# Kernel optimization log

Measured on AMD Instinct MI355X. Metric: run time of the kernel, lower is better.

Reference implementation:

```python
import jax, jax.numpy as jnp
import numpy as np

B, S, D = 2, 2048, 2048
H, HD = 16, 128
F = 8192
LC = 512
EPS = 1e-6


def _linear_params(k, din, dout):
    k1, k2 = jax.random.split(k)
    w = jax.random.normal(k1, (din, dout), jnp.float32) * 0.02
    b = jax.random.normal(k2, (dout,), jnp.float32) * 0.02
    return w, b


def setup_inputs() -> dict:
    key = jax.random.key(0)
    ks = jax.random.split(key, 20)
    inp = {}
    inp["x"] = jax.random.normal(ks[0], (B, S, D), jnp.float32)
    inp["e"] = jax.random.normal(ks[1], (B, 6, D), jnp.float32) * 0.1
    inp["context"] = jax.random.normal(ks[2], (B, LC, D), jnp.float32)
    # per-token rotary angles [S, HD//2] (Wan builds such a table from 3D grid)
    inp["freqs"] = jax.random.uniform(ks[3], (S, HD // 2), jnp.float32) * (2.0 * np.pi)
    inp["modulation"] = jax.random.normal(ks[4], (1, 6, D), jnp.float32) / np.sqrt(D)
    names = ["sq", "sk", "sv", "so", "cq", "ck", "cv", "co"]
    for i, nm in enumerate(names):
        w, b = _linear_params(ks[5 + i], D, D)
        inp[nm + "_w"], inp[nm + "_b"] = w, b
    inp["f1_w"], inp["f1_b"] = _linear_params(ks[13], D, F)
    inp["f2_w"], inp["f2_b"] = _linear_params(ks[14], F, D)
    inp["snq"] = jnp.ones((D,), jnp.float32)
    inp["snk"] = jnp.ones((D,), jnp.float32)
    inp["cnq"] = jnp.ones((D,), jnp.float32)
    inp["cnk"] = jnp.ones((D,), jnp.float32)
    return inp


def _rmsnorm(x, w):
    # WanRMSNorm: x * rsqrt(mean(x^2) + eps) * weight
    return x * jax.lax.rsqrt(jnp.mean(x * x, axis=-1, keepdims=True) + EPS) * w


def _layernorm(x):
    # elementwise_affine=False LayerNorm
    m = jnp.mean(x, axis=-1, keepdims=True)
    v = jnp.mean((x - m) ** 2, axis=-1, keepdims=True)
    return (x - m) * jax.lax.rsqrt(v + EPS)


def _rope(x, ang):
    # x: [B, S, H, HD]; ang: [S, HD//2]; adjacent pairs rotated (view_as_complex)
    c = jnp.cos(ang)[None, :, None, :]
    s = jnp.sin(ang)[None, :, None, :]
    xr, xi = x[..., 0::2], x[..., 1::2]
    out = jnp.stack([xr * c - xi * s, xr * s + xi * c], axis=-1)
    return out.reshape(x.shape)


def _attn(q, k, v):
    # q: [B,Sq,H,HD], k/v: [B,Sk,H,HD] -> [B,Sq,H,HD]
    scores = jnp.einsum("bqhd,bkhd->bhqk", q, k) / np.sqrt(HD)
    probs = jax.nn.softmax(scores, axis=-1)
    return jnp.einsum("bhqk,bkhd->bqhd", probs, v)


def reference(x, e, context, freqs, modulation,
              sq_w, sq_b, sk_w, sk_b, sv_w, sv_b, so_w, so_b, snq, snk,
              cq_w, cq_b, ck_w, ck_b, cv_w, cv_b, co_w, co_b, cnq, cnk,
              f1_w, f1_b, f2_w, f2_b):
    em = modulation + e  # [B,6,D]
    e0, e1, e2, e3, e4, e5 = [em[:, i:i + 1, :] for i in range(6)]

    # self-attention with AdaLN modulation
    tx = _layernorm(x) * (1.0 + e1) + e0
    q = _rmsnorm(tx @ sq_w + sq_b, snq).reshape(B, S, H, HD)
    k = _rmsnorm(tx @ sk_w + sk_b, snk).reshape(B, S, H, HD)
    v = (tx @ sv_w + sv_b).reshape(B, S, H, HD)
    q, k = _rope(q, freqs), _rope(k, freqs)
    y = _attn(q, k, v).reshape(B, S, D) @ so_w + so_b
    x = x + y * e2

    # cross-attention (norm3 = Identity since cross_attn_norm=False)
    q = _rmsnorm(x @ cq_w + cq_b, cnq).reshape(B, S, H, HD)
    k = _rmsnorm(context @ ck_w + ck_b, cnk).reshape(B, LC, H, HD)
    v = (context @ cv_w + cv_b).reshape(B, LC, H, HD)
    x = x + (_attn(q, k, v).reshape(B, S, D) @ co_w + co_b)

    # FFN with AdaLN modulation
    tx = _layernorm(x) * (1.0 + e4) + e3
    y = jax.nn.gelu(tx @ f1_w + f1_b, approximate=True) @ f2_w + f2_b
    x = x + y * e5
    return x
```

## Files before the change

kernel.cpp:

```cpp
#include <hip/hip_runtime.h>
#include <hip/hip_bf16.h>

using bf16 = __hip_bfloat16;
typedef __attribute__((ext_vector_type(8))) short bf16x8;
typedef __attribute__((ext_vector_type(4))) float f32x4;
typedef const __attribute__((address_space(1))) unsigned int* gp_t;
typedef __attribute__((address_space(3))) unsigned int* sp_t;

#define B_   2
#define S_   2048
#define D_   2048
#define H_   16
#define HD_  128
#define F_   8192
#define LC_  512
#define ESTRIDE (6*D_)

__device__ __forceinline__ float bsum4(float v, float* rs) {
  #pragma unroll
  for (int o = 32; o; o >>= 1) v += __shfl_down(v, o, 64);
  int lane = threadIdx.x & 63, w = threadIdx.x >> 6;
  if (!lane) rs[w] = v;
  __syncthreads();
  float r = rs[0] + rs[1] + rs[2] + rs[3];
  __syncthreads();
  return r;
}
__device__ __forceinline__ float bmax4(float v, float* rs) {
  #pragma unroll
  for (int o = 32; o; o >>= 1) v = fmaxf(v, __shfl_down(v, o, 64));
  int lane = threadIdx.x & 63, w = threadIdx.x >> 6;
  if (!lane) rs[w] = v;
  __syncthreads();
  float r = fmaxf(fmaxf(rs[0], rs[1]), fmaxf(rs[2], rs[3]));
  __syncthreads();
  return r;
}

template <int N>
__device__ __forceinline__ void vmwait() {
  asm volatile("s_waitcnt vmcnt(%0)" :: "n"(N) : "memory");
}
__device__ __forceinline__ void vmnone() {}

__global__ void k_addmod(const float* __restrict__ e, const float* __restrict__ mod,
                         float* __restrict__ em) {
  int i = blockIdx.x * 256 + threadIdx.x;
  em[i] = e[i] + mod[i % (6 * D_)];
}

__global__ void k_f2b(const float* __restrict__ in, bf16* __restrict__ out) {
  int i = blockIdx.x * 256 + threadIdx.x;
  out[i] = __float2bfloat16(in[i]);
}

__global__ void k_copy_f32(const float* __restrict__ in, float* __restrict__ out) {
  int i = blockIdx.x * 256 + threadIdx.x;
  out[i] = in[i];
}

__global__ void k_tr_f2b(const float* __restrict__ in, bf16* __restrict__ out,
                         int K, int N) {
  __shared__ float tile[64][65];
  int kb = blockIdx.y << 6, nb = blockIdx.x << 6;
  int x = threadIdx.x & 63, y = threadIdx.x >> 6;
  #pragma unroll
  for (int r = y; r < 64; r += 4) tile[r][x] = in[(size_t)(kb + r) * N + nb + x];
  __syncthreads();
  #pragma unroll
  for (int r = y; r < 64; r += 4)
    out[(size_t)(nb + r) * K + kb + x] = __float2bfloat16(tile[x][r]);
}

__global__ void k_tr_b2b(const bf16* __restrict__ in, bf16* __restrict__ out,
                         int R, int C, long long sIn, long long sOut) {
  in  += (long long)blockIdx.z * sIn;
  out += (long long)blockIdx.z * sOut;
  __shared__ bf16 tile[64][65];
  int rb = blockIdx.y << 6, cb = blockIdx.x << 6;
  int x = threadIdx.x & 63, y = threadIdx.x >> 6;
  #pragma unroll
  for (int r = y; r < 64; r += 4) tile[r][x] = in[(size_t)(rb + r) * C + cb + x];
  __syncthreads();
  #pragma unroll
  for (int r = y; r < 64; r += 4) out[(size_t)(cb + r) * R + rb + x] = tile[x][r];
}

__global__ void k_ln_mod(const float* __restrict__ x, const float* __restrict__ em,
                         int i0, int i1, bf16* __restrict__ out, int s_per_b) {
  __shared__ float rs[4];
  int row = blockIdx.x, t = threadIdx.x;
  int b = row / s_per_b;
  const float* xr = x + (size_t)row * D_;
  float vals[8], s = 0.f, ss = 0.f;
  #pragma unroll
  for (int j = 0; j < 8; j++) {
    float v = xr[t + j * 256];
    vals[j] = v; s += v; ss += v * v;
  }
  s  = bsum4(s, rs);
  ss = bsum4(ss, rs);
  float mean = s * (1.f / D_);
  float var  = ss * (1.f / D_) - mean * mean;
  float inv  = rsqrtf(var + 1e-6f);
  const float* e0 = em + ((size_t)b * 6 + i0) * D_;
  const float* e1 = em + ((size_t)b * 6 + i1) * D_;
  bf16* orow = out + (size_t)row * D_;
  #pragma unroll
  for (int j = 0; j < 8; j++) {
    int c = t + j * 256;
    orow[c] = __float2bfloat16((vals[j] - mean) * inv * (1.f + e1[c]) + e0[c]);
  }
}

__global__ void k_rms_rope(bf16* __restrict__ buf, const float* __restrict__ w,
                           const float* __restrict__ freqs, int do_rope, int s_per_b) {
  __shared__ float rs[4];
  int row = blockIdx.x, t = threadIdx.x;
  bf16* pr = buf + (size_t)row * D_;
  float4 raw = *(const float4*)(pr + (size_t)t * 8);
  bf16* hb = (bf16*)&raw;
  float v[8], ss = 0.f;
  #pragma unroll
  for (int j = 0; j < 8; j++) { v[j] = __bfloat162float(hb[j]); ss += v[j] * v[j]; }
  ss = bsum4(ss, rs);
  float inv = rsqrtf(ss * (1.f / D_) + 1e-6f);
  int base = t * 8;
  #pragma unroll
  for (int j = 0; j < 8; j++) v[j] = v[j] * inv * w[base + j];
  if (do_rope) {
    int s = row % s_per_b;
    const float* fr = freqs + (size_t)s * (HD_ / 2) + ((base & (HD_ - 1)) >> 1);
    #pragma unroll
    for (int p = 0; p < 4; p++) {
      float ang = fr[p];
      float c = cosf(ang), sn = sinf(ang);
      float xr = v[2 * p], xi = v[2 * p + 1];
      v[2 * p]     = xr * c - xi * sn;
      v[2 * p + 1] = xr * sn + xi * c;
    }
  }
  float4 ow; bf16* ho = (bf16*)&ow;
  #pragma unroll
  for (int j = 0; j < 8; j++) ho[j] = __float2bfloat16(v[j]);
  *(float4*)(pr + (size_t)t * 8) = ow;
}

template <int EPT>
__global__ void k_softmax(bf16* __restrict__ buf, int N) {
  __shared__ float rs[4];
  int row = blockIdx.x, t = threadIdx.x;
  bf16* pr = buf + (size_t)row * N;
  float v[EPT], mx = -1e30f;
  #pragma unroll
  for (int j = 0; j < EPT; j++) { v[j] = __bfloat162float(pr[t + j * 256]); mx = fmaxf(mx, v[j]); }
  mx = bmax4(mx, rs);
  float s = 0.f;
  #pragma unroll
  for (int j = 0; j < EPT; j++) { v[j] = __expf(v[j] - mx); s += v[j]; }
  s = bsum4(s, rs);
  float invs = 1.f / s;
  #pragma unroll
  for (int j = 0; j < EPT; j++) pr[t + j * 256] = __float2bfloat16(v[j] * invs);
}

__device__ __forceinline__ void xcd_swizzle(int& bx, int& by) {
  int nx = gridDim.x, ny = gridDim.y;
  if ((nx & 7) == 0) {
    int flat = by * nx + bx;
    int xcd = flat & 7;
    int idx = flat >> 3;
    int sx = nx >> 3;
    bx = xcd * sx + (idx % sx);
    by = idx / sx;
    (void)ny;
  }
}

template <int EPI>
__global__ __launch_bounds__(256) void gemm_bt(
    const bf16* __restrict__ A, int lda, long long sA,
    const bf16* __restrict__ Bt, int ldb, long long sB,
    const float* __restrict__ bias,
    bf16* __restrict__ Cb, int ldc, long long sCb,
    float* __restrict__ Cf, const float* __restrict__ Xin,
    float scale, const float* __restrict__ evec, int s_per_b,
    int K) {
  __shared__ __align__(16) bf16 As[128][32];
  __shared__ __align__(16) bf16 Bs[128][32];
  const int z = blockIdx.z;
  A  += (long long)z * sA;
  Bt += (long long)z * sB;
  int bx = blockIdx.x, by = blockIdx.y;
  xcd_swizzle(bx, by);
  const int m0 = by * 128, n0 = bx * 128;
  const int t = threadIdx.x;
  const int w = t >> 6, lane = t & 63;
  const int wrow = (w >> 1) * 64, wcol = (w & 1) * 64;
  const int quad = lane >> 4, l16 = lane & 15;

  f32x4 zero = {0.f, 0.f, 0.f, 0.f};
  f32x4 acc[4][4];
  #pragma unroll
  for (int i = 0; i < 4; i++)
    #pragma unroll
    for (int j = 0; j < 4; j++) acc[i][j] = zero;

  for (int k0 = 0; k0 < K; k0 += 32) {
    #pragma unroll
    for (int i = 0; i < 2; i++) {
      int c = t + i * 256;
      int r = c >> 2, col = (c & 3) * 8;
      __builtin_amdgcn_global_load_lds(
          (gp_t)(A + (size_t)(m0 + r) * lda + k0 + col),
          (sp_t)(&As[0][0] + (size_t)(w * 64 + i * 256) * 8), 16, 0, 0);
      __builtin_amdgcn_global_load_lds(
          (gp_t)(Bt + (size_t)(n0 + r) * ldb + k0 + col),
          (sp_t)(&Bs[0][0] + (size_t)(w * 64 + i * 256) * 8), 16, 0, 0);
    }
    __syncthreads();
    bf16x8 af[4], bfr[4];
    #pragma unroll
    for (int mi = 0; mi < 4; mi++) af[mi]  = *(const bf16x8*)(&As[wrow + mi * 16 + l16][quad * 8]);
    #pragma unroll
    for (int ni = 0; ni < 4; ni++) bfr[ni] = *(const bf16x8*)(&Bs[wcol + ni * 16 + l16][quad * 8]);
    #pragma unroll
    for (int mi = 0; mi < 4; mi++)
      #pragma unroll
      for (int ni = 0; ni < 4; ni++)
        acc[mi][ni] = __builtin_amdgcn_mfma_f32_16x16x32_bf16(af[mi], bfr[ni], acc[mi][ni], 0, 0, 0);
    __syncthreads();
  }

  #pragma unroll
  for (int mi = 0; mi < 4; mi++) {
    #pragma unroll
    for (int r = 0; r < 4; r++) {
      int gm = m0 + wrow + mi * 16 + quad * 4 + r;
      #pragma unroll
      for (int ni = 0; ni < 4; ni++) {
        int gn = n0 + wcol + ni * 16 + l16;
        float v = acc[mi][ni][r];
        if (EPI == 0) {
          if (bias) v += bias[gn];
          Cb[(long long)z * sCb + (size_t)gm * ldc + gn] = __float2bfloat16(v);
        } else if (EPI == 1) {
          Cb[(long long)z * sCb + (size_t)gm * ldc + gn] = __float2bfloat16(v * scale);
        }
      }
    }
  }
}

__global__ __launch_bounds__(256) void gemm64(
    const bf16* __restrict__ A, int lda, long long sA,
    const bf16* __restrict__ Bt, int ldb, long long sB,
    bf16* __restrict__ Cb, int ldc, long long sCb,
    int K) {
  __shared__ __align__(16) bf16 As[64][32];
  __shared__ __align__(16) bf16 Bs[64][32];
  const int z = blockIdx.z;
  A  += (long long)z * sA;
  Bt += (long long)z * sB;
  const int m0 = blockIdx.y * 64, n0 = blockIdx.x * 64;
  const int t = threadIdx.x;
  const int w = t >> 6, lane = t & 63;
  const int wrow = (w >> 1) * 32, wcol = (w & 1) * 32;
  const int quad = lane >> 4, l16 = lane & 15;

  f32x4 zero = {0.f, 0.f, 0.f, 0.f};
  f32x4 acc[2][2];
  #pragma unroll
  for (int i = 0; i < 2; i++)
    #pragma unroll
    for (int j = 0; j < 2; j++) acc[i][j] = zero;

  for (int k0 = 0; k0 < K; k0 += 32) {
    {
      int r = t >> 2, col = (t & 3) * 8;
      __builtin_amdgcn_global_load_lds(
          (gp_t)(A + (size_t)(m0 + r) * lda + k0 + col),
          (sp_t)(&As[0][0] + (size_t)(w * 64) * 8), 16, 0, 0);
      __builtin_amdgcn_global_load_lds(
          (gp_t)(Bt + (size_t)(n0 + r) * ldb + k0 + col),
          (sp_t)(&Bs[0][0] + (size_t)(w * 64) * 8), 16, 0, 0);
    }
    __syncthreads();
    bf16x8 af[2], bfr[2];
    #pragma unroll
    for (int mi = 0; mi < 2; mi++) af[mi]  = *(const bf16x8*)(&As[wrow + mi * 16 + l16][quad * 8]);
    #pragma unroll
    for (int ni = 0; ni < 2; ni++) bfr[ni] = *(const bf16x8*)(&Bs[wcol + ni * 16 + l16][quad * 8]);
    #pragma unroll
    for (int mi = 0; mi < 2; mi++)
      #pragma unroll
      for (int ni = 0; ni < 2; ni++)
        acc[mi][ni] = __builtin_amdgcn_mfma_f32_16x16x32_bf16(af[mi], bfr[ni], acc[mi][ni], 0, 0, 0);
    __syncthreads();
  }

  #pragma unroll
  for (int mi = 0; mi < 2; mi++) {
    #pragma unroll
    for (int r = 0; r < 4; r++) {
      int gm = m0 + wrow + mi * 16 + quad * 4 + r;
      #pragma unroll
      for (int ni = 0; ni < 2; ni++) {
        int gn = n0 + wcol + ni * 16 + l16;
        Cb[(long long)z * sCb + (size_t)gm * ldc + gn] = __float2bfloat16(acc[mi][ni][r]);
      }
    }
  }
}

__device__ __forceinline__ void stage_half2(const bf16* P, int ld, int grow0,
                                            int k0, bf16* ldshalf, int w, int lane) {
  #pragma unroll
  for (int j = 0; j < 2; j++) {
    int offw = j * 8192 + w * 1024;
    int off  = offw + lane * 16;
    int r = off >> 7;
    int chunk = ((off >> 4) & 7) ^ (r & 7);
    __builtin_amdgcn_global_load_lds(
        (gp_t)(P + (size_t)(grow0 + r) * ld + k0 + chunk * 8),
        (sp_t)((char*)ldshalf + offw), 16, 0, 0);
  }
}
__device__ __forceinline__ void stage_half1(const bf16* P, int ld, int grow0,
                                            int k0, bf16* ldshalf, int w, int lane) {
  int offw = w * 1024;
  int off  = offw + lane * 16;
  int r = off >> 7;
  int chunk = ((off >> 4) & 7) ^ (r & 7);
  __builtin_amdgcn_global_load_lds(
      (gp_t)(P + (size_t)(grow0 + r) * ld + k0 + chunk * 8),
      (sp_t)((char*)ldshalf + offw), 16, 0, 0);
}

#define PHASE(AH, BH, CURB, STAGE_STMT, VM_STMT) do {                          \
    __builtin_amdgcn_sched_barrier(0);                                         \
    bf16x8 af[FI][2], bv[2][2];                                                \
    const char* aB = (const char*)&As[(CURB)][0][0];                           \
    const char* bB = (const char*)&Bs[(CURB)][0][0];                           \
    _Pragma("unroll")                                                          \
    for (int fi = 0; fi < FI; fi++) {                                          \
      int ar = wm * RH + (AH) * 128 + fi * 16 + l16;                           \
      _Pragma("unroll")                                                        \
      for (int ks = 0; ks < 2; ks++)                                           \
        af[fi][ks] = *(const bf16x8*)(aB + ar * 128 +                          \
                                      ((64 * ks + 16 * quad) ^ swz));          \
    }                                                                          \
    _Pragma("unroll")                                                          \
    for (int fj = 0; fj < 2; fj++) {                                           \
      int br = wn * 32 + (BH) * CHALF + fj * 16 + l16;                         \
      _Pragma("unroll")                                                        \
      for (int ks = 0; ks < 2; ks++)                                           \
        bv[fj][ks] = *(const bf16x8*)(bB + br * 128 +                          \
                                      ((64 * ks + 16 * quad) ^ swz));          \
    }                                                                          \
    STAGE_STMT;                                                                \
    VM_STMT;                                                                   \
    __builtin_amdgcn_s_barrier();                                              \
    __builtin_amdgcn_s_setprio(1);                                             \
    _Pragma("unroll")                                                          \
    for (int fi = 0; fi < FI; fi++)                                            \
      _Pragma("unroll")                                                        \
      for (int fj = 0; fj < 2; fj++)                                           \
        _Pragma("unroll")                                                      \
        for (int ks = 0; ks < 2; ks++)                                         \
          acc[(AH)][(BH)][fi][fj] = __builtin_amdgcn_mfma_f32_16x16x32_bf16(   \
              af[fi][ks], bv[fj][ks], acc[(AH)][(BH)][fi][fj], 0, 0, 0);       \
    __builtin_amdgcn_s_setprio(0);                                             \
    __builtin_amdgcn_s_barrier();                                              \
  } while (0)

template <int EPI, int BN, int WM, int WN>
__global__ __launch_bounds__(512, 2) void gemm256(
    const bf16* __restrict__ A, int lda, long long sA,
    const bf16* __restrict__ Bt, int ldb, long long sB,
    const float* __restrict__ bias,
    bf16* __restrict__ Cb, int ldc, long long sCb,
    float* __restrict__ Cf, const float* __restrict__ Xin,
    float scale, const float* __restrict__ evec, int s_per_b, int K) {
  constexpr int RH = 256 / (WM * 2);
  constexpr int FI = RH / 16;
  constexpr int CHALF = BN / 2;
  constexpr int LB = (BN == 256) ? 2 : 1;
  constexpr int PRO_V = 2 + LB;
  constexpr int P2_V = (BN == 256) ? 8 : 6;
  constexpr int P4_V = (BN == 256) ? 6 : 5;

  __shared__ __align__(16) bf16 As[2][256][64];
  __shared__ __align__(16) bf16 Bs[2][BN][64];

  const int z = blockIdx.z;
  A  += (long long)z * sA;
  Bt += (long long)z * sB;
  int bx = blockIdx.x, by = blockIdx.y;
  xcd_swizzle(bx, by);
  const int m0 = by * 256, n0 = bx * BN;
  const int t = threadIdx.x;
  const int w = t >> 6, lane = t & 63;
  const int wm = w / WN, wn = w % WN;
  const int quad = lane >> 4, l16 = lane & 15;
  const int swz = (l16 & 7) << 4;

  f32x4 zero = {0.f, 0.f, 0.f, 0.f};
  f32x4 acc[2][2][FI][2];
  #pragma unroll
  for (int a = 0; a < 2; a++)
    #pragma unroll
    for (int b = 0; b < 2; b++)
      #pragma unroll
      for (int i = 0; i < FI; i++)
        #pragma unroll
        for (int j = 0; j < 2; j++) acc[a][b][i][j] = zero;

  const int NT = K >> 6;

  stage_half2(A, lda, m0,        0, &As[0][0][0],     w, lane);
  if (LB == 2) stage_half2(Bt, ldb, n0,        0, &Bs[0][0][0],     w, lane);
  else         stage_half1(Bt, ldb, n0,        0, &Bs[0][0][0],     w, lane);
  if (LB == 2) stage_half2(Bt, ldb, n0 + CHALF, 0, &Bs[0][CHALF][0], w, lane);
  else         stage_half1(Bt, ldb, n0 + CHALF, 0, &Bs[0][CHALF][0], w, lane);
  stage_half2(A, lda, m0 + 128,  0, &As[0][128][0],   w, lane);
  stage_half2(A, lda, m0,       64, &As[1][0][0],     w, lane);
  if (LB == 2) stage_half2(Bt, ldb, n0 + CHALF, 64, &Bs[1][CHALF][0], w, lane);
  else         stage_half1(Bt, ldb, n0 + CHALF, 64, &Bs[1][CHALF][0], w, lane);
  vmwait<PRO_V>();
  __builtin_amdgcn_s_barrier();

  for (int tt = 0; tt < NT; tt++) {
    const int cur = tt & 1, nxt = cur ^ 1;
    const int w1 = (tt + 1 < NT) ? tt + 1 : 0;
    const int w2 = (tt + 2 < NT) ? tt + 2 : tt + 2 - NT;
    PHASE(0, 0, cur,
          (LB == 2 ? stage_half2(Bt, ldb, n0, w1 * 64, &Bs[nxt][0][0], w, lane)
                   : stage_half1(Bt, ldb, n0, w1 * 64, &Bs[nxt][0][0], w, lane)),
          vmnone());
    PHASE(0, 1, cur,
          (stage_half2(A, lda, m0 + 128, w1 * 64, &As[nxt][128][0], w, lane)),
          vmwait<P2_V>());
    PHASE(1, 1, cur,
          (stage_half2(A, lda, m0, w2 * 64, &As[cur][0][0], w, lane)),
          vmnone());
    PHASE(1, 0, cur,
          (LB == 2 ? stage_half2(Bt, ldb, n0 + CHALF, w2 * 64, &Bs[cur][CHALF][0], w, lane)
                   : stage_half1(Bt, ldb, n0 + CHALF, w2 * 64, &Bs[cur][CHALF][0], w, lane)),
          vmwait<P4_V>());
  }
  asm volatile("s_waitcnt vmcnt(0)" ::: "memory");

  #pragma unroll
  for (int ah = 0; ah < 2; ah++)
    #pragma unroll
    for (int fi = 0; fi < FI; fi++)
      #pragma unroll
      for (int r = 0; r < 4; r++) {
        int gm = m0 + wm * RH + ah * 128 + fi * 16 + quad * 4 + r;
        #pragma unroll
        for (int bh = 0; bh < 2; bh++)
          #pragma unroll
          for (int fj = 0; fj < 2; fj++) {
            int gn = n0 + wn * 32 + bh * CHALF + fj * 16 + l16;
            float v = acc[ah][bh][fi][fj][r];
            if (EPI == 0) {
              if (bias) v += bias[gn];
              Cb[(long long)z * sCb + (size_t)gm * ldc + gn] = __float2bfloat16(v);
            } else if (EPI == 3) {
              v += bias[gn];
              float u = 1.5957691216057308f * (v + 0.044715f * v * v * v);
              float g = v / (1.f + __expf(-u));
              Cb[(long long)z * sCb + (size_t)gm * ldc + gn] = __float2bfloat16(g);
            } else {
              v += bias[gn];
              if (evec) v *= evec[(size_t)(gm / s_per_b) * ESTRIDE + gn];
              float o = Xin[(size_t)gm * ldc + gn] + v;
              Cf[(size_t)gm * ldc + gn] = o;
              if (Cb) Cb[(size_t)gm * ldc + gn] = __float2bfloat16(o);
            }
          }
      }
  (void)scale;
}

extern "C" void kernel_launch(void* const* d_in, const int* in_sizes, int n_in,
                              void* d_out, int out_size, void* d_ws, size_t ws_size,
                              hipStream_t stream) {
  const float* x     = (const float*)d_in[0];
  const float* e     = (const float*)d_in[1];
  const float* ctx   = (const float*)d_in[2];
  const float* freqs = (const float*)d_in[3];
  const float* modu  = (const float*)d_in[4];
  const float* sq_w = (const float*)d_in[5];  const float* sq_b = (const float*)d_in[6];
  const float* sk_w = (const float*)d_in[7];  const float* sk_b = (const float*)d_in[8];
  const float* sv_w = (const float*)d_in[9];  const float* sv_b = (const float*)d_in[10];
  const float* so_w = (const float*)d_in[11]; const float* so_b = (const float*)d_in[12];
  const float* cq_w = (const float*)d_in[13]; const float* cq_b = (const float*)d_in[14];
  const float* ck_w = (const float*)d_in[15]; const float* ck_b = (const float*)d_in[16];
  const float* cv_w = (const float*)d_in[17]; const float* cv_b = (const float*)d_in[18];
  const float* co_w = (const float*)d_in[19]; const float* co_b = (const float*)d_in[20];
  const float* f1_w = (const float*)d_in[21]; const float* f1_b = (const float*)d_in[22];
  const float* f2_w = (const float*)d_in[23]; const float* f2_b = (const float*)d_in[24];
  const float* snq  = (const float*)d_in[25]; const float* snk  = (const float*)d_in[26];
  const float* cnq  = (const float*)d_in[27]; const float* cnk  = (const float*)d_in[28];
  float* out = (float*)d_out;

  const size_t MD = (size_t)B_ * S_ * D_;

  char* W = (char*)d_ws;
  size_t off = 0;
  auto alloc = [&](size_t bytes) -> char* {
    char* p = W + off; off += (bytes + 255) & ~(size_t)255; return p;
  };
  float* em  = (float*)alloc((size_t)B_ * 6 * D_ * 4);
  bf16* wT   = (bf16*)alloc((size_t)F_ * D_ * 2);
  bf16* vb   = (bf16*)alloc(MD * 2);
  bf16* tx   = (bf16*)alloc(MD * 2);
  bf16* qb   = (bf16*)alloc(MD * 2);
  bf16* kb   = (bf16*)alloc(MD * 2);
  bf16* vt   = (bf16*)alloc(MD * 2);
  bf16* attnout = (bf16*)alloc(MD * 2);
  bf16* ctxb = (bf16*)alloc((size_t)B_ * LC_ * D_ * 2);
  bf16* kc   = (bf16*)alloc((size_t)B_ * LC_ * D_ * 2);
  bf16* vc   = (bf16*)alloc((size_t)B_ * LC_ * D_ * 2);
  bf16* vtc  = (bf16*)alloc((size_t)B_ * LC_ * D_ * 2);
  bf16* scores8 = wT;
  bf16* scoresC = wT;
  bf16* mid = qb;
  if (off > ws_size) {
    k_copy_f32<<<(int)(MD / 256), 256, 0, stream>>>(x, out);
    return;
  }

  const float qk_scale = 0.08838834764831845f;

  k_addmod<<<(B_ * 6 * D_) / 256, 256, 0, stream>>>(e, modu, em);
  k_f2b<<<(B_ * LC_ * D_) / 256, 256, 0, stream>>>(ctx, ctxb);

  k_ln_mod<<<B_ * S_, 256, 0, stream>>>(x, em, 0, 1, tx, S_);
  k_tr_f2b<<<dim3(D_ / 64, D_ / 64), 256, 0, stream>>>(sq_w, wT, D_, D_);
  gemm256<0, 128, 4, 2><<<dim3(16, 16, 1), 512, 0, stream>>>(tx, D_, 0, wT, D_, 0, sq_b,
      qb, D_, 0, nullptr, nullptr, 1.f, nullptr, S_, D_);
  k_tr_f2b<<<dim3(D_ / 64, D_ / 64), 256, 0, stream>>>(sk_w, wT, D_, D_);
  gemm256<0, 128, 4, 2><<<dim3(16, 16, 1), 512, 0, stream>>>(tx, D_, 0, wT, D_, 0, sk_b,
      kb, D_, 0, nullptr, nullptr, 1.f, nullptr, S_, D_);
  k_tr_f2b<<<dim3(D_ / 64, D_ / 64), 256, 0, stream>>>(sv_w, wT, D_, D_);
  gemm256<0, 128, 4, 2><<<dim3(16, 16, 1), 512, 0, stream>>>(tx, D_, 0, wT, D_, 0, sv_b,
      vb, D_, 0, nullptr, nullptr, 1.f, nullptr, S_, D_);
  k_rms_rope<<<B_ * S_, 256, 0, stream>>>(qb, snq, freqs, 1, S_);
  k_rms_rope<<<B_ * S_, 256, 0, stream>>>(kb, snk, freqs, 1, S_);
  k_tr_b2b<<<dim3(D_ / 64, S_ / 64, B_), 256, 0, stream>>>(vb, vt, S_, D_,
      (long long)S_ * D_, (long long)D_ * S_);

  for (int b = 0; b < B_; b++) {
    for (int hc = 0; hc < 2; hc++) {
      const int h0 = hc * 8;
      const bf16* Aq = qb + (size_t)b * S_ * D_ + h0 * HD_;
      const bf16* Bk = kb + (size_t)b * S_ * D_ + h0 * HD_;
      gemm_bt<1><<<dim3(16, 16, 8), 256, 0, stream>>>(Aq, D_, HD_, Bk, D_, HD_, nullptr,
          scores8, S_, (long long)S_ * S_, nullptr, nullptr, qk_scale, nullptr, S_, HD_);
      k_softmax<8><<<8 * S_, 256, 0, stream>>>(scores8, S_);
      const bf16* Bv = vt + ((size_t)b * D_ + h0 * HD_) * S_;
      gemm64<<<dim3(2, 32, 8), 256, 0, stream>>>(scores8, S_, (long long)S_ * S_,
          Bv, S_, (long long)HD_ * S_,
          attnout + (size_t)b * S_ * D_ + h0 * HD_, D_, HD_, S_);
    }
  }
  k_tr_f2b<<<dim3(D_ / 64, D_ / 64), 256, 0, stream>>>(so_w, wT, D_, D_);
  gemm256<2, 128, 4, 2><<<dim3(16, 16, 1), 512, 0, stream>>>(attnout, D_, 0, wT, D_, 0, so_b,
      tx, D_, 0, out, x, 1.f, em + 2 * D_, S_, D_);

  k_tr_f2b<<<dim3(D_ / 64, D_ / 64), 256, 0, stream>>>(cq_w, wT, D_, D_);
  gemm256<0, 128, 4, 2><<<dim3(16, 16, 1), 512, 0, stream>>>(tx, D_, 0, wT, D_, 0, cq_b,
      qb, D_, 0, nullptr, nullptr, 1.f, nullptr, S_, D_);
  k_rms_rope<<<B_ * S_, 256, 0, stream>>>(qb, cnq, nullptr, 0, S_);
  k_tr_f2b<<<dim3(D_ / 64, D_ / 64), 256, 0, stream>>>(ck_w, wT, D_, D_);
  gemm_bt<0><<<dim3(16, 8, 1), 256, 0, stream>>>(ctxb, D_, 0, wT, D_, 0, ck_b,
      kc, D_, 0, nullptr, nullptr, 1.f, nullptr, S_, D_);
  k_rms_rope<<<B_ * LC_, 256, 0, stream>>>(kc, cnk, nullptr, 0, S_);
  k_tr_f2b<<<dim3(D_ / 64, D_ / 64), 256, 0, stream>>>(cv_w, wT, D_, D_);
  gemm_bt<0><<<dim3(16, 8, 1), 256, 0, stream>>>(ctxb, D_, 0, wT, D_, 0, cv_b,
      vc, D_, 0, nullptr, nullptr, 1.f, nullptr, S_, D_);
  k_tr_b2b<<<dim3(D_ / 64, LC_ / 64, B_), 256, 0, stream>>>(vc, vtc, LC_, D_,
      (long long)LC_ * D_, (long long)D_ * LC_);

  for (int b = 0; b < B_; b++) {
    gemm_bt<1><<<dim3(4, 16, 16), 256, 0, stream>>>(qb + (size_t)b * S_ * D_, D_, HD_,
        kc + (size_t)b * LC_ * D_, D_, HD_, nullptr,
        scoresC, LC_, (long long)S_ * LC_, nullptr, nullptr, qk_scale, nullptr, S_, HD_);
    k_softmax<2><<<16 * S_, 256, 0, stream>>>(scoresC, LC_);
    gemm64<<<dim3(2, 32, 16), 256, 0, stream>>>(scoresC, LC_, (long long)S_ * LC_,
        vtc + (size_t)b * D_ * LC_, LC_, (long long)HD_ * LC_,
        attnout + (size_t)b * S_ * D_, D_, HD_, LC_);
  }
  k_tr_f2b<<<dim3(D_ / 64, D_ / 64), 256, 0, stream>>>(co_w, wT, D_, D_);
  gemm256<2, 128, 4, 2><<<dim3(16, 16, 1), 512, 0, stream>>>(attnout, D_, 0, wT, D_, 0, co_b,
      nullptr, D_, 0, out, out, 1.f, nullptr, S_, D_);

  k_ln_mod<<<B_ * S_, 256, 0, stream>>>(out, em, 3, 4, tx, S_);
  k_tr_f2b<<<dim3(F_ / 64, D_ / 64), 256, 0, stream>>>(f1_w, wT, D_, F_);
  gemm256<3, 256, 2, 4><<<dim3(32, 16, 1), 512, 0, stream>>>(tx, D_, 0, wT, D_, 0, f1_b,
      mid, F_, 0, nullptr, nullptr, 1.f, nullptr, S_, D_);
  k_tr_f2b<<<dim3(D_ / 64, F_ / 64), 256, 0, stream>>>(f2_w, wT, F_, D_);
  gemm256<2, 128, 4, 2><<<dim3(16, 16, 1), 512, 0, stream>>>(mid, F_, 0, wT, F_, 0, f2_b,
      nullptr, D_, 0, out, out, 1.f, em + 5 * D_, S_, F_);
}
```

Baseline: 1.860 ms.

## Fuse QKV projections into one GEMM and unify gemm256 on 256x256 tiles

```diff
diff --git a/kernel.cpp b/kernel.cpp
--- a/kernel.cpp
+++ b/kernel.cpp
@@ -14,6 +14,7 @@
 #define HD_  128
 #define F_   8192
 #define LC_  512
+#define QKVC 6144
 #define ESTRIDE (6*D_)
 
 __device__ __forceinline__ float bsum4(float v, float* rs) {
@@ -59,6 +60,12 @@
   out[i] = in[i];
 }
 
+__global__ void k_cat3(const float* __restrict__ a, const float* __restrict__ b,
+                       const float* __restrict__ c, float* __restrict__ o) {
+  int i = blockIdx.x * 256 + threadIdx.x;
+  o[i] = (i < D_) ? a[i] : (i < 2 * D_ ? b[i - D_] : c[i - 2 * D_]);
+}
+
 __global__ void k_tr_f2b(const float* __restrict__ in, bf16* __restrict__ out,
                          int K, int N) {
   __shared__ float tile[64][65];
@@ -73,14 +80,14 @@
 }
 
 __global__ void k_tr_b2b(const bf16* __restrict__ in, bf16* __restrict__ out,
-                         int R, int C, long long sIn, long long sOut) {
+                         int R, int C, int ldin, long long sIn, long long sOut) {
   in  += (long long)blockIdx.z * sIn;
   out += (long long)blockIdx.z * sOut;
   __shared__ bf16 tile[64][65];
   int rb = blockIdx.y << 6, cb = blockIdx.x << 6;
   int x = threadIdx.x & 63, y = threadIdx.x >> 6;
   #pragma unroll
-  for (int r = y; r < 64; r += 4) tile[r][x] = in[(size_t)(rb + r) * C + cb + x];
+  for (int r = y; r < 64; r += 4) tile[r][x] = in[(size_t)(rb + r) * ldin + cb + x];
   __syncthreads();
   #pragma unroll
   for (int r = y; r < 64; r += 4) out[(size_t)(cb + r) * R + rb + x] = tile[x][r];
@@ -113,11 +120,11 @@
   }
 }
 
-__global__ void k_rms_rope(bf16* __restrict__ buf, const float* __restrict__ w,
+__global__ void k_rms_rope(bf16* __restrict__ buf, int ld, const float* __restrict__ w,
                            const float* __restrict__ freqs, int do_rope, int s_per_b) {
   __shared__ float rs[4];
   int row = blockIdx.x, t = threadIdx.x;
-  bf16* pr = buf + (size_t)row * D_;
+  bf16* pr = buf + (size_t)row * ld;
   float4 raw = *(const float4*)(pr + (size_t)t * 8);
   bf16* hb = (bf16*)&raw;
   float v[8], ss = 0.f;
@@ -164,16 +171,17 @@
   for (int j = 0; j < EPT; j++) pr[t + j * 256] = __float2bfloat16(v[j] * invs);
 }
 
-__device__ __forceinline__ void xcd_swizzle(int& bx, int& by) {
+__device__ __forceinline__ void xcd_map(int& bx, int& by, int mode) {
   int nx = gridDim.x, ny = gridDim.y;
-  if ((nx & 7) == 0) {
-    int flat = by * nx + bx;
-    int xcd = flat & 7;
-    int idx = flat >> 3;
-    int sx = nx >> 3;
+  int flat = by * nx + bx;
+  if (mode == 1 && (nx & 7) == 0) {
+    int xcd = flat & 7, idx = flat >> 3, sx = nx >> 3;
     bx = xcd * sx + (idx % sx);
     by = idx / sx;
-    (void)ny;
+  } else if (mode == 2 && (ny & 7) == 0) {
+    int xcd = flat & 7, idx = flat >> 3, sy = ny >> 3;
+    bx = idx % nx;
+    by = xcd * sy + idx / nx;
   }
 }
 
@@ -183,16 +191,22 @@
     const bf16* __restrict__ Bt, int ldb, long long sB,
     const float* __restrict__ bias,
     bf16* __restrict__ Cb, int ldc, long long sCb,
-    float* __restrict__ Cf, const float* __restrict__ Xin,
-    float scale, const float* __restrict__ evec, int s_per_b,
-    int K) {
+    float scale, int K) {
   __shared__ __align__(16) bf16 As[128][32];
   __shared__ __align__(16) bf16 Bs[128][32];
   const int z = blockIdx.z;
   A  += (long long)z * sA;
   Bt += (long long)z * sB;
   int bx = blockIdx.x, by = blockIdx.y;
-  xcd_swizzle(bx, by);
+  {
+    int nx = gridDim.x;
+    if ((nx & 7) == 0) {
+      int flat = by * nx + bx;
+      int xcd = flat & 7, idx = flat >> 3, sx = nx >> 3;
+      bx = xcd * sx + (idx % sx);
+      by = idx / sx;
+    }
+  }
   const int m0 = by * 128, n0 = bx * 128;
   const int t = threadIdx.x;
   const int w = t >> 6, lane = t & 63;
@@ -313,8 +327,8 @@
   }
 }
 
-__device__ __forceinline__ void stage_half2(const bf16* P, int ld, int grow0,
-                                            int k0, bf16* ldshalf, int w, int lane) {
+__device__ __forceinline__ void stage_half(const bf16* P, int ld, int grow0,
+                                           int k0, bf16* ldshalf, int w, int lane) {
   #pragma unroll
   for (int j = 0; j < 2; j++) {
     int offw = j * 8192 + w * 1024;
@@ -326,25 +340,15 @@
         (sp_t)((char*)ldshalf + offw), 16, 0, 0);
   }
 }
-__device__ __forceinline__ void stage_half1(const bf16* P, int ld, int grow0,
-                                            int k0, bf16* ldshalf, int w, int lane) {
-  int offw = w * 1024;
-  int off  = offw + lane * 16;
-  int r = off >> 7;
-  int chunk = ((off >> 4) & 7) ^ (r & 7);
-  __builtin_amdgcn_global_load_lds(
-      (gp_t)(P + (size_t)(grow0 + r) * ld + k0 + chunk * 8),
-      (sp_t)((char*)ldshalf + offw), 16, 0, 0);
-}
 
 #define PHASE(AH, BH, CURB, STAGE_STMT, VM_STMT) do {                          \
     __builtin_amdgcn_sched_barrier(0);                                         \
-    bf16x8 af[FI][2], bv[2][2];                                                \
+    bf16x8 af[4][2], bv[2][2];                                                 \
     const char* aB = (const char*)&As[(CURB)][0][0];                           \
     const char* bB = (const char*)&Bs[(CURB)][0][0];                           \
     _Pragma("unroll")                                                          \
-    for (int fi = 0; fi < FI; fi++) {                                          \
-      int ar = wm * RH + (AH) * 128 + fi * 16 + l16;                           \
+    for (int fi = 0; fi < 4; fi++) {                                           \
+      int ar = wm * 64 + (AH) * 128 + fi * 16 + l16;                           \
       _Pragma("unroll")                                                        \
       for (int ks = 0; ks < 2; ks++)                                           \
         af[fi][ks] = *(const bf16x8*)(aB + ar * 128 +                          \
@@ -352,7 +356,7 @@
     }                                                                          \
     _Pragma("unroll")                                                          \
     for (int fj = 0; fj < 2; fj++) {                                           \
-      int br = wn * 32 + (BH) * CHALF + fj * 16 + l16;                         \
+      int br = wn * 32 + (BH) * 128 + fj * 16 + l16;                           \
       _Pragma("unroll")                                                        \
       for (int ks = 0; ks < 2; ks++)                                           \
         bv[fj][ks] = *(const bf16x8*)(bB + br * 128 +                          \
@@ -363,7 +367,7 @@
     __builtin_amdgcn_s_barrier();                                              \
     __builtin_amdgcn_s_setprio(1);                                             \
     _Pragma("unroll")                                                          \
-    for (int fi = 0; fi < FI; fi++)                                            \
+    for (int fi = 0; fi < 4; fi++)                                             \
       _Pragma("unroll")                                                        \
       for (int fj = 0; fj < 2; fj++)                                           \
         _Pragma("unroll")                                                      \
@@ -374,60 +378,49 @@
     __builtin_amdgcn_s_barrier();                                              \
   } while (0)
 
-template <int EPI, int BN, int WM, int WN>
+template <int EPI>
 __global__ __launch_bounds__(512, 2) void gemm256(
     const bf16* __restrict__ A, int lda, long long sA,
     const bf16* __restrict__ Bt, int ldb, long long sB,
     const float* __restrict__ bias,
     bf16* __restrict__ Cb, int ldc, long long sCb,
     float* __restrict__ Cf, const float* __restrict__ Xin,
-    float scale, const float* __restrict__ evec, int s_per_b, int K) {
-  constexpr int RH = 256 / (WM * 2);
-  constexpr int FI = RH / 16;
-  constexpr int CHALF = BN / 2;
-  constexpr int LB = (BN == 256) ? 2 : 1;
-  constexpr int PRO_V = 2 + LB;
-  constexpr int P2_V = (BN == 256) ? 8 : 6;
-  constexpr int P4_V = (BN == 256) ? 6 : 5;
-
+    const float* __restrict__ evec, int s_per_b, int K, int swzmode) {
   __shared__ __align__(16) bf16 As[2][256][64];
-  __shared__ __align__(16) bf16 Bs[2][BN][64];
+  __shared__ __align__(16) bf16 Bs[2][256][64];
 
   const int z = blockIdx.z;
   A  += (long long)z * sA;
   Bt += (long long)z * sB;
   int bx = blockIdx.x, by = blockIdx.y;
-  xcd_swizzle(bx, by);
-  const int m0 = by * 256, n0 = bx * BN;
+  xcd_map(bx, by, swzmode);
+  const int m0 = by * 256, n0 = bx * 256;
   const int t = threadIdx.x;
   const int w = t >> 6, lane = t & 63;
-  const int wm = w / WN, wn = w % WN;
+  const int wm = w >> 2, wn = w & 3;
   const int quad = lane >> 4, l16 = lane & 15;
   const int swz = (l16 & 7) << 4;
 
   f32x4 zero = {0.f, 0.f, 0.f, 0.f};
-  f32x4 acc[2][2][FI][2];
+  f32x4 acc[2][2][4][2];
   #pragma unroll
   for (int a = 0; a < 2; a++)
     #pragma unroll
     for (int b = 0; b < 2; b++)
       #pragma unroll
-      for (int i = 0; i < FI; i++)
+      for (int i = 0; i < 4; i++)
         #pragma unroll
         for (int j = 0; j < 2; j++) acc[a][b][i][j] = zero;
 
   const int NT = K >> 6;
 
-  stage_half2(A, lda, m0,        0, &As[0][0][0],     w, lane);
-  if (LB == 2) stage_half2(Bt, ldb, n0,        0, &Bs[0][0][0],     w, lane);
-  else         stage_half1(Bt, ldb, n0,        0, &Bs[0][0][0],     w, lane);
-  if (LB == 2) stage_half2(Bt, ldb, n0 + CHALF, 0, &Bs[0][CHALF][0], w, lane);
-  else         stage_half1(Bt, ldb, n0 + CHALF, 0, &Bs[0][CHALF][0], w, lane);
-  stage_half2(A, lda, m0 + 128,  0, &As[0][128][0],   w, lane);
-  stage_half2(A, lda, m0,       64, &As[1][0][0],     w, lane);
-  if (LB == 2) stage_half2(Bt, ldb, n0 + CHALF, 64, &Bs[1][CHALF][0], w, lane);
-  else         stage_half1(Bt, ldb, n0 + CHALF, 64, &Bs[1][CHALF][0], w, lane);
-  vmwait<PRO_V>();
+  stage_half(A,  lda, m0,       0, &As[0][0][0],   w, lane);
+  stage_half(Bt, ldb, n0,       0, &Bs[0][0][0],   w, lane);
+  stage_half(Bt, ldb, n0 + 128, 0, &Bs[0][128][0], w, lane);
+  stage_half(A,  lda, m0 + 128, 0, &As[0][128][0], w, lane);
+  stage_half(A,  lda, m0,      64, &As[1][0][0],   w, lane);
+  stage_half(Bt, ldb, n0 + 128, 64, &Bs[1][128][0], w, lane);
+  vmwait<4>();
   __builtin_amdgcn_s_barrier();
 
   for (int tt = 0; tt < NT; tt++) {
@@ -435,34 +428,32 @@
     const int w1 = (tt + 1 < NT) ? tt + 1 : 0;
     const int w2 = (tt + 2 < NT) ? tt + 2 : tt + 2 - NT;
     PHASE(0, 0, cur,
-          (LB == 2 ? stage_half2(Bt, ldb, n0, w1 * 64, &Bs[nxt][0][0], w, lane)
-                   : stage_half1(Bt, ldb, n0, w1 * 64, &Bs[nxt][0][0], w, lane)),
+          (stage_half(Bt, ldb, n0, w1 * 64, &Bs[nxt][0][0], w, lane)),
           vmnone());
     PHASE(0, 1, cur,
-          (stage_half2(A, lda, m0 + 128, w1 * 64, &As[nxt][128][0], w, lane)),
-          vmwait<P2_V>());
+          (stage_half(A, lda, m0 + 128, w1 * 64, &As[nxt][128][0], w, lane)),
+          vmwait<8>());
     PHASE(1, 1, cur,
-          (stage_half2(A, lda, m0, w2 * 64, &As[cur][0][0], w, lane)),
+          (stage_half(A, lda, m0, w2 * 64, &As[cur][0][0], w, lane)),
           vmnone());
     PHASE(1, 0, cur,
-          (LB == 2 ? stage_half2(Bt, ldb, n0 + CHALF, w2 * 64, &Bs[cur][CHALF][0], w, lane)
-                   : stage_half1(Bt, ldb, n0 + CHALF, w2 * 64, &Bs[cur][CHALF][0], w, lane)),
-          vmwait<P4_V>());
+          (stage_half(Bt, ldb, n0 + 128, w2 * 64, &Bs[cur][128][0], w, lane)),
+          vmwait<6>());
   }
   asm volatile("s_waitcnt vmcnt(0)" ::: "memory");
 
   #pragma unroll
   for (int ah = 0; ah < 2; ah++)
     #pragma unroll
-    for (int fi = 0; fi < FI; fi++)
+    for (int fi = 0; fi < 4; fi++)
       #pragma unroll
       for (int r = 0; r < 4; r++) {
-        int gm = m0 + wm * RH + ah * 128 + fi * 16 + quad * 4 + r;
+        int gm = m0 + wm * 64 + ah * 128 + fi * 16 + quad * 4 + r;
         #pragma unroll
         for (int bh = 0; bh < 2; bh++)
           #pragma unroll
           for (int fj = 0; fj < 2; fj++) {
-            int gn = n0 + wn * 32 + bh * CHALF + fj * 16 + l16;
+            int gn = n0 + wn * 32 + bh * 128 + fj * 16 + l16;
             float v = acc[ah][bh][fi][fj][r];
             if (EPI == 0) {
               if (bias) v += bias[gn];
@@ -481,7 +472,6 @@
             }
           }
       }
-  (void)scale;
 }
 
 extern "C" void kernel_launch(void* const* d_in, const int* in_sizes, int n_in,
@@ -515,19 +505,19 @@
   };
   float* em  = (float*)alloc((size_t)B_ * 6 * D_ * 4);
   bf16* wT   = (bf16*)alloc((size_t)F_ * D_ * 2);
-  bf16* vb   = (bf16*)alloc(MD * 2);
   bf16* tx   = (bf16*)alloc(MD * 2);
-  bf16* qb   = (bf16*)alloc(MD * 2);
-  bf16* kb   = (bf16*)alloc(MD * 2);
+  bf16* qkv  = (bf16*)alloc((size_t)B_ * S_ * QKVC * 2);
   bf16* vt   = (bf16*)alloc(MD * 2);
   bf16* attnout = (bf16*)alloc(MD * 2);
   bf16* ctxb = (bf16*)alloc((size_t)B_ * LC_ * D_ * 2);
   bf16* kc   = (bf16*)alloc((size_t)B_ * LC_ * D_ * 2);
   bf16* vc   = (bf16*)alloc((size_t)B_ * LC_ * D_ * 2);
   bf16* vtc  = (bf16*)alloc((size_t)B_ * LC_ * D_ * 2);
-  bf16* scores8 = wT;
+  float* bqkv = (float*)alloc((size_t)3 * D_ * 4);
+  bf16* scores4 = wT;
   bf16* scoresC = wT;
-  bf16* mid = qb;
+  bf16* qb2 = vt;
+  bf16* mid = qkv;
   if (off > ws_size) {
     k_copy_f32<<<(int)(MD / 256), 256, 0, stream>>>(x, out);
     return;
@@ -537,72 +527,69 @@
 
   k_addmod<<<(B_ * 6 * D_) / 256, 256, 0, stream>>>(e, modu, em);
   k_f2b<<<(B_ * LC_ * D_) / 256, 256, 0, stream>>>(ctx, ctxb);
+  k_cat3<<<(3 * D_) / 256, 256, 0, stream>>>(sq_b, sk_b, sv_b, bqkv);
 
   k_ln_mod<<<B_ * S_, 256, 0, stream>>>(x, em, 0, 1, tx, S_);
   k_tr_f2b<<<dim3(D_ / 64, D_ / 64), 256, 0, stream>>>(sq_w, wT, D_, D_);
-  gemm256<0, 128, 4, 2><<<dim3(16, 16, 1), 512, 0, stream>>>(tx, D_, 0, wT, D_, 0, sq_b,
-      qb, D_, 0, nullptr, nullptr, 1.f, nullptr, S_, D_);
-  k_tr_f2b<<<dim3(D_ / 64, D_ / 64), 256, 0, stream>>>(sk_w, wT, D_, D_);
-  gemm256<0, 128, 4, 2><<<dim3(16, 16, 1), 512, 0, stream>>>(tx, D_, 0, wT, D_, 0, sk_b,
-      kb, D_, 0, nullptr, nullptr, 1.f, nullptr, S_, D_);
-  k_tr_f2b<<<dim3(D_ / 64, D_ / 64), 256, 0, stream>>>(sv_w, wT, D_, D_);
-  gemm256<0, 128, 4, 2><<<dim3(16, 16, 1), 512, 0, stream>>>(tx, D_, 0, wT, D_, 0, sv_b,
-      vb, D_, 0, nullptr, nullptr, 1.f, nullptr, S_, D_);
-  k_rms_rope<<<B_ * S_, 256, 0, stream>>>(qb, snq, freqs, 1, S_);
-  k_rms_rope<<<B_ * S_, 256, 0, stream>>>(kb, snk, freqs, 1, S_);
-  k_tr_b2b<<<dim3(D_ / 64, S_ / 64, B_), 256, 0, stream>>>(vb, vt, S_, D_,
-      (long long)S_ * D_, (long long)D_ * S_);
+  k_tr_f2b<<<dim3(D_ / 64, D_ / 64), 256, 0, stream>>>(sk_w, wT + (size_t)D_ * D_, D_, D_);
+  k_tr_f2b<<<dim3(D_ / 64, D_ / 64), 256, 0, stream>>>(sv_w, wT + (size_t)2 * D_ * D_, D_, D_);
+  gemm256<0><<<dim3(QKVC / 256, 16, 1), 512, 0, stream>>>(tx, D_, 0, wT, D_, 0, bqkv,
+      qkv, QKVC, 0, nullptr, nullptr, nullptr, S_, D_, 2);
+  k_rms_rope<<<B_ * S_, 256, 0, stream>>>(qkv, QKVC, snq, freqs, 1, S_);
+  k_rms_rope<<<B_ * S_, 256, 0, stream>>>(qkv + D_, QKVC, snk, freqs, 1, S_);
+  k_tr_b2b<<<dim3(D_ / 64, S_ / 64, B_), 256, 0, stream>>>(qkv + 2 * D_, vt, S_, D_, QKVC,
+      (long long)S_ * QKVC, (long long)D_ * S_);
 
   for (int b = 0; b < B_; b++) {
-    for (int hc = 0; hc < 2; hc++) {
-      const int h0 = hc * 8;
-      const bf16* Aq = qb + (size_t)b * S_ * D_ + h0 * HD_;
-      const bf16* Bk = kb + (size_t)b * S_ * D_ + h0 * HD_;
-      gemm_bt<1><<<dim3(16, 16, 8), 256, 0, stream>>>(Aq, D_, HD_, Bk, D_, HD_, nullptr,
-          scores8, S_, (long long)S_ * S_, nullptr, nullptr, qk_scale, nullptr, S_, HD_);
-      k_softmax<8><<<8 * S_, 256, 0, stream>>>(scores8, S_);
+    for (int hc = 0; hc < 4; hc++) {
+      const int h0 = hc * 4;
+      const bf16* Aq = qkv + (size_t)b * S_ * QKVC + h0 * HD_;
+      const bf16* Bk = qkv + (size_t)b * S_ * QKVC + D_ + h0 * HD_;
+      gemm_bt<1><<<dim3(16, 16, 4), 256, 0, stream>>>(Aq, QKVC, HD_, Bk, QKVC, HD_, nullptr,
+          scores4, S_, (long long)S_ * S_, qk_scale, HD_);
+      k_softmax<8><<<4 * S_, 256, 0, stream>>>(scores4, S_);
       const bf16* Bv = vt + ((size_t)b * D_ + h0 * HD_) * S_;
-      gemm64<<<dim3(2, 32, 8), 256, 0, stream>>>(scores8, S_, (long long)S_ * S_,
+      gemm64<<<dim3(2, 32, 4), 256, 0, stream>>>(scores4, S_, (long long)S_ * S_,
           Bv, S_, (long long)HD_ * S_,
           attnout + (size_t)b * S_ * D_ + h0 * HD_, D_, HD_, S_);
     }
   }
   k_tr_f2b<<<dim3(D_ / 64, D_ / 64), 256, 0, stream>>>(so_w, wT, D_, D_);
-  gemm256<2, 128, 4, 2><<<dim3(16, 16, 1), 512, 0, stream>>>(attnout, D_, 0, wT, D_, 0, so_b,
-      tx, D_, 0, out, x, 1.f, em + 2 * D_, S_, D_);
+  gemm256<2><<<dim3(8, 16, 1), 512, 0, stream>>>(attnout, D_, 0, wT, D_, 0, so_b,
+      tx, D_, 0, out, x, em + 2 * D_, S_, D_, 2);
 
   k_tr_f2b<<<dim3(D_ / 64, D_ / 64), 256, 0, stream>>>(cq_w, wT, D_, D_);
-  gemm256<0, 128, 4, 2><<<dim3(16, 16, 1), 512, 0, stream>>>(tx, D_, 0, wT, D_, 0, cq_b,
-      qb, D_, 0, nullptr, nullptr, 1.f, nullptr, S_, D_);
-  k_rms_rope<<<B_ * S_, 256, 0, stream>>>(qb, cnq, nullptr, 0, S_);
+  gemm256<0><<<dim3(8, 16, 1), 512, 0, stream>>>(tx, D_, 0, wT, D_, 0, cq_b,
+      qb2, D_, 0, nullptr, nullptr, nullptr, S_, D_, 2);
+  k_rms_rope<<<B_ * S_, 256, 0, stream>>>(qb2, D_, cnq, nullptr, 0, S_);
   k_tr_f2b<<<dim3(D_ / 64, D_ / 64), 256, 0, stream>>>(ck_w, wT, D_, D_);
   gemm_bt<0><<<dim3(16, 8, 1), 256, 0, stream>>>(ctxb, D_, 0, wT, D_, 0, ck_b,
-      kc, D_, 0, nullptr, nullptr, 1.f, nullptr, S_, D_);
-  k_rms_rope<<<B_ * LC_, 256, 0, stream>>>(kc, cnk, nullptr, 0, S_);
+      kc, D_, 0, 1.f, D_);
+  k_rms_rope<<<B_ * LC_, 256, 0, stream>>>(kc, D_, cnk, nullptr, 0, S_);
   k_tr_f2b<<<dim3(D_ / 64, D_ / 64), 256, 0, stream>>>(cv_w, wT, D_, D_);
   gemm_bt<0><<<dim3(16, 8, 1), 256, 0, stream>>>(ctxb, D_, 0, wT, D_, 0, cv_b,
-      vc, D_, 0, nullptr, nullptr, 1.f, nullptr, S_, D_);
-  k_tr_b2b<<<dim3(D_ / 64, LC_ / 64, B_), 256, 0, stream>>>(vc, vtc, LC_, D_,
+      vc, D_, 0, 1.f, D_);
+  k_tr_b2b<<<dim3(D_ / 64, LC_ / 64, B_), 256, 0, stream>>>(vc, vtc, LC_, D_, D_,
       (long long)LC_ * D_, (long long)D_ * LC_);
 
   for (int b = 0; b < B_; b++) {
-    gemm_bt<1><<<dim3(4, 16, 16), 256, 0, stream>>>(qb + (size_t)b * S_ * D_, D_, HD_,
+    gemm_bt<1><<<dim3(4, 16, 16), 256, 0, stream>>>(qb2 + (size_t)b * S_ * D_, D_, HD_,
         kc + (size_t)b * LC_ * D_, D_, HD_, nullptr,
-        scoresC, LC_, (long long)S_ * LC_, nullptr, nullptr, qk_scale, nullptr, S_, HD_);
+        scoresC, LC_, (long long)S_ * LC_, qk_scale, HD_);
     k_softmax<2><<<16 * S_, 256, 0, stream>>>(scoresC, LC_);
     gemm64<<<dim3(2, 32, 16), 256, 0, stream>>>(scoresC, LC_, (long long)S_ * LC_,
         vtc + (size_t)b * D_ * LC_, LC_, (long long)HD_ * LC_,
         attnout + (size_t)b * S_ * D_, D_, HD_, LC_);
   }
   k_tr_f2b<<<dim3(D_ / 64, D_ / 64), 256, 0, stream>>>(co_w, wT, D_, D_);
-  gemm256<2, 128, 4, 2><<<dim3(16, 16, 1), 512, 0, stream>>>(attnout, D_, 0, wT, D_, 0, co_b,
-      nullptr, D_, 0, out, out, 1.f, nullptr, S_, D_);
+  gemm256<2><<<dim3(8, 16, 1), 512, 0, stream>>>(attnout, D_, 0, wT, D_, 0, co_b,
+      nullptr, D_, 0, out, out, nullptr, S_, D_, 2);
 
   k_ln_mod<<<B_ * S_, 256, 0, stream>>>(out, em, 3, 4, tx, S_);
   k_tr_f2b<<<dim3(F_ / 64, D_ / 64), 256, 0, stream>>>(f1_w, wT, D_, F_);
-  gemm256<3, 256, 2, 4><<<dim3(32, 16, 1), 512, 0, stream>>>(tx, D_, 0, wT, D_, 0, f1_b,
-      mid, F_, 0, nullptr, nullptr, 1.f, nullptr, S_, D_);
+  gemm256<3><<<dim3(32, 16, 1), 512, 0, stream>>>(tx, D_, 0, wT, D_, 0, f1_b,
+      mid, F_, 0, nullptr, nullptr, nullptr, S_, D_, 1);
   k_tr_f2b<<<dim3(D_ / 64, F_ / 64), 256, 0, stream>>>(f2_w, wT, F_, D_);
-  gemm256<2, 128, 4, 2><<<dim3(16, 16, 1), 512, 0, stream>>>(mid, F_, 0, wT, F_, 0, f2_b,
-      nullptr, D_, 0, out, out, 1.f, em + 5 * D_, S_, F_);
-}
+  gemm256<2><<<dim3(8, 16, 1), 512, 0, stream>>>(mid, F_, 0, wT, F_, 0, f2_b,
+      nullptr, D_, 0, out, out, em + 5 * D_, S_, F_, 2);
+}
```

Result: slower. 2.128 ms (+14.4%).
